# Kernel optimization log

Measured on AMD Instinct MI355X. Metric: run time of the kernel, lower is better.

Reference implementation:

```python
import jax, jax.numpy as jnp
import numpy as np

B = 1024
IN_SIZ = 16384
OUT_SIZ = 16384
C = 8          # channel_siz
NLVL = 10
IFS = IN_SIZ // 2 ** NLVL                                   # 16, in_filter_siz
KLVL = min(int(np.floor(np.log2(OUT_SIZ / 2))), NLVL)       # 10
OFS = OUT_SIZ // 2 ** KLVL                                  # 16, out_filter_siz
STD = 0.9


def setup_inputs() -> dict:
    key = jax.random.key(0)
    ks = jax.random.split(key, 2 * NLVL + 3)
    inp = {}
    inp["x"] = jax.random.normal(ks[0], (B, IN_SIZ, 1), jnp.float32)
    inp["in_filter"] = jax.random.normal(ks[1], (IFS, 1, C), jnp.float32) * STD
    inp["in_bias"] = jnp.zeros((C,), jnp.float32)
    for lvl in range(1, NLVL + 1):
        k = 2 ** lvl
        inp[f"W{lvl}"] = jax.random.normal(ks[2 * lvl], (k, 2, C, C), jnp.float32) * STD
        inp[f"b{lvl}"] = jnp.zeros((k, C), jnp.float32)
    inp["fea_dense"] = jax.random.normal(ks[-1], (2 ** KLVL, C, OFS), jnp.float32) * STD
    return inp


def _level(v, W, b):
    # v: [Kp, B, L, C] parent branches; W: [2*Kp, 2, C, C]; b: [2*Kp, C]
    # kernel-2 stride-2 conv1d: out[t] = relu(x[2t] @ W[0] + x[2t+1] @ W[1] + b)
    Kp, Bn, L, Cc = v.shape
    xp = v.reshape(Kp, Bn, L // 2, 2, Cc)
    xr = jnp.repeat(xp, 2, axis=0)  # child itk reads parent itk // 2
    y = jnp.einsum('kbtsc,kscd->kbtd', xr, W) + b[:, None, None, :]
    return jax.nn.relu(y)


def reference(x, in_filter, in_bias,
              W1, b1, W2, b2, W3, b3, W4, b4, W5, b5,
              W6, b6, W7, b7, W8, b8, W9, b9, W10, b10,
              fea_dense):
    Ws = [W1, W2, W3, W4, W5, W6, W7, W8, W9, W10]
    bs = [b1, b2, b3, b4, b5, b6, b7, b8, b9, b10]
    Bn = x.shape[0]
    # input conv1d: kernel=IFS, stride=IFS (non-overlapping) == blocked matmul
    xin = x[..., 0].reshape(Bn, 2 ** NLVL, IFS)                       # [B, 1024, 16]
    v = jax.nn.relu(jnp.einsum('bnf,fc->bnc', xin, in_filter[:, 0, :]) + in_bias)
    v = v[None]                                                        # [1, B, 1024, C]
    for lvl in range(NLVL):  # klvl == nlvl: all levels branch (tree doubling)
        v = _level(v, Ws[lvl], bs[lvl])
    # v: [2^klvl, B, 1, C] -> per-branch dense feature map
    out = jnp.einsum('kbc,kcf->bkf', v[:, :, 0, :], fea_dense)         # [B, 1024, OFS]
    return out.reshape(Bn, OUT_SIZ, 1)
```

## Files before the change

### kernel.cpp

```cpp
#include <hip/hip_runtime.h>

struct PrepPtrs { const float* W[7]; const float* Bv[7]; const float* F; const float* fb; };

__device__ __forceinline__ int cz(int c) { return c ^ ((c >> 3) & 3); }

__device__ __forceinline__ float4 relu4(float4 a) {
  return make_float4(fmaxf(a.x,0.f), fmaxf(a.y,0.f), fmaxf(a.z,0.f), fmaxf(a.w,0.f));
}
__device__ __forceinline__ void fma4(float4& acc, float s, const float4& wv) {
  acc.x = fmaf(s, wv.x, acc.x); acc.y = fmaf(s, wv.y, acc.y);
  acc.z = fmaf(s, wv.z, acc.z); acc.w = fmaf(s, wv.w, acc.w);
}

__global__ void bfly_prep(PrepPtrs P, float* __restrict__ wt) {
  int e = blockIdx.x * 256 + threadIdx.x;
  if (e >= 510 * 68) return;
  int ent = e / 68, r = e % 68, dd = r & 3;
  float v; int dst;
  if (ent < 62) {
    dst = ent * 80 + r;
    if (ent < 60) {
      int lvl, base;
      if (ent < 4)       { lvl = 1; base = 0;  }
      else if (ent < 12) { lvl = 2; base = 4;  }
      else if (ent < 28) { lvl = 3; base = 12; }
      else               { lvl = 4; base = 28; }
      int k = (ent - base) >> 1, th = ent & 1;
      if (r < 64) { int s = r >> 5, c = (r >> 2) & 7;
        v = P.W[lvl-1][k*128 + s*64 + c*8 + th*4 + dd]; }
      else v = P.Bv[lvl-1][k*8 + th*4 + dd];
    } else {
      int th = ent - 60;
      if (r < 64) { int f = r >> 2; v = P.F[f*8 + th*4 + dd]; }
      else v = P.fb[th*4 + dd];
    }
  } else {
    int eb = ent - 62;
    int q = eb / 56, rem = eb % 56;
    int lvl, Kl, base;
    if (rem < 8)       { lvl = 5; Kl = 4;  base = 0;  }
    else if (rem < 24) { lvl = 6; Kl = 8;  base = 8;  }
    else               { lvl = 7; Kl = 16; base = 24; }
    int rr = rem - base, lk = rr >> 1, th = rr & 1;
    int kg = q * Kl + lk;
    if (r < 64) { int s = r >> 5, c = (r >> 2) & 7;
      v = P.W[lvl-1][kg*128 + s*64 + c*8 + th*4 + dd]; }
    else v = P.Bv[lvl-1][kg*8 + th*4 + dd];
    dst = 4960 + eb * 80 + r;
  }
  wt[dst] = v;
}

template<int L>
__device__ __forceinline__ void ka_level(const float4* __restrict__ src,
                                         float4* __restrict__ dst,
                                         const float4* __restrict__ wt4,
                                         int lane, int wq, int th) {
  constexpr int Kc = 1 << L, Tc = 1024 >> L;
  constexpr int entBase = (Kc - 2) * 2;
  constexpr int kIters = (L <= 2) ? 1 : (1 << (L - 2));
  constexpr int tIters = 4 / kIters;
#pragma unroll
  for (int ik = 0; ik < kIters; ++ik) {
    int k;
    if constexpr (L == 1) k = wq & 1;
    else if constexpr (L == 2) k = wq;
    else k = wq + 4 * ik;
    const float4* e4 = wt4 + (entBase + k * 2 + th) * 20;
    const int kp = k >> 1;
#pragma unroll
    for (int it = 0; it < tIters; ++it) {
      int t;
      if constexpr (L == 1) t = lane + (wq >> 1) * 64 + it * 128;
      else if constexpr (L == 2) t = lane + it * 64;
      else if constexpr (L == 3) t = lane + it * 64;
      else t = lane;
      int pb = kp * (2 * Tc) + 2 * t;
      float4 A0 = src[cz(pb)],        C0 = src[cz(pb + 1)];
      float4 A1 = src[cz(pb + 1024)], C1 = src[cz(pb + 1025)];
      float4 a = e4[16];
      fma4(a, A0.x, e4[0]);  fma4(a, A0.y, e4[1]);  fma4(a, A0.z, e4[2]);  fma4(a, A0.w, e4[3]);
      fma4(a, A1.x, e4[4]);  fma4(a, A1.y, e4[5]);  fma4(a, A1.z, e4[6]);  fma4(a, A1.w, e4[7]);
      fma4(a, C0.x, e4[8]);  fma4(a, C0.y, e4[9]);  fma4(a, C0.z, e4[10]); fma4(a, C0.w, e4[11]);
      fma4(a, C1.x, e4[12]); fma4(a, C1.y, e4[13]); fma4(a, C1.z, e4[14]); fma4(a, C1.w, e4[15]);
      dst[cz(th * 1024 + k * Tc + t)] = relu4(a);
    }
  }
}

__global__ __launch_bounds__(512, 2) void bfly_ka(
    const float* __restrict__ x, const float* __restrict__ wt,
    float* __restrict__ st1)
{
  __shared__ float4 sA[2048], sB[2048];
  const int tid = threadIdx.x, b = blockIdx.x;
  const int lane = tid & 63;
  const int wv = __builtin_amdgcn_readfirstlane(tid >> 6);
  const int th = wv & 1, wq = wv >> 1;
  const float4* wt4 = (const float4*)wt;

  {
    const float4* e4 = wt4 + (60 + th) * 20;
    const float* xb = x + (size_t)b * 16384;
#pragma unroll
    for (int i = 0; i < 4; ++i) {
      int n = lane + wq * 64 + i * 256;
      const float4* xr = (const float4*)(xb + n * 16);
      float4 x0 = xr[0], x1 = xr[1], x2 = xr[2], x3 = xr[3];
      float4 a = e4[16];
      fma4(a, x0.x, e4[0]);  fma4(a, x0.y, e4[1]);  fma4(a, x0.z, e4[2]);  fma4(a, x0.w, e4[3]);
      fma4(a, x1.x, e4[4]);  fma4(a, x1.y, e4[5]);  fma4(a, x1.z, e4[6]);  fma4(a, x1.w, e4[7]);
      fma4(a, x2.x, e4[8]);  fma4(a, x2.y, e4[9]);  fma4(a, x2.z, e4[10]); fma4(a, x2.w, e4[11]);
      fma4(a, x3.x, e4[12]); fma4(a, x3.y, e4[13]); fma4(a, x3.z, e4[14]); fma4(a, x3.w, e4[15]);
      sA[cz(th * 1024 + n)] = relu4(a);
    }
  }
  __syncthreads();
  ka_level<1>(sA, sB, wt4, lane, wq, th); __syncthreads();
  ka_level<2>(sB, sA, wt4, lane, wq, th); __syncthreads();
  ka_level<3>(sA, sB, wt4, lane, wq, th); __syncthreads();
  ka_level<4>(sB, sA, wt4, lane, wq, th); __syncthreads();

  float4* o4 = (float4*)st1;
#pragma unroll
  for (int it = 0; it < 4; ++it) {
    int o = tid + it * 512;
    int t4 = o & 63, k4 = (o >> 6) & 15, h = o >> 10;
    o4[((size_t)(h * 16 + k4) * 1024 + b) * 64 + t4] = sA[cz(o)];
  }
}

template<int LV>
__device__ __forceinline__ void kb_level(const float4* __restrict__ src,
                                         float4* __restrict__ dst,
                                         const float4* __restrict__ wb4,
                                         int lane, int wv) {
  constexpr int Kc = 1 << (LV - 3);
  constexpr int Tc = 128 / Kc;
  constexpr int Tp = 256 / Kc;
  constexpr int entB = (LV == 5) ? 0 : (LV == 6) ? 8 : 24;
  constexpr int kIters = Kc / 4;
  constexpr int nIt = 4 / kIters;
  const int th = wv & 1, w2 = wv >> 1;
#pragma unroll
  for (int ik = 0; ik < kIters; ++ik) {
    const int lk = w2 + 4 * ik;
    const float4* e4 = wb4 + (entB + lk * 2 + th) * 20;
    const int lkp = lk >> 1;
#pragma unroll
    for (int it = 0; it < nIt; ++it) {
      int t, bb;
      if constexpr (LV == 5)      { t = lane & 31; bb = (lane >> 5) + it * 2; }
      else if constexpr (LV == 6) { t = lane & 15; bb = (lane >> 4) + it * 4; }
      else                        { t = lane & 7;  bb = lane >> 3; }
      int pb = bb * 256 + lkp * Tp + 2 * t;
      float4 A0 = src[cz(pb)],       C0 = src[cz(pb + 1)];
      float4 A1 = src[cz(pb + 128)], C1 = src[cz(pb + 129)];
      float4 a = e4[16];
      fma4(a, A0.x, e4[0]);  fma4(a, A0.y, e4[1]);  fma4(a, A0.z, e4[2]);  fma4(a, A0.w, e4[3]);
      fma4(a, A1.x, e4[4]);  fma4(a, A1.y, e4[5]);  fma4(a, A1.z, e4[6]);  fma4(a, A1.w, e4[7]);
      fma4(a, C0.x, e4[8]);  fma4(a, C0.y, e4[9]);  fma4(a, C0.z, e4[10]); fma4(a, C0.w, e4[11]);
      fma4(a, C1.x, e4[12]); fma4(a, C1.y, e4[13]); fma4(a, C1.z, e4[14]); fma4(a, C1.w, e4[15]);
      dst[cz(bb * 256 + th * 128 + lk * Tc + t)] = relu4(a);
    }
  }
}

__global__ __launch_bounds__(512, 2) void bfly_kb(
    const float* __restrict__ st1, const float* __restrict__ wt,
    float* __restrict__ st2)
{
  __shared__ float4 s0[2048], s1[2048];
  const int tid = threadIdx.x;
  const int q = blockIdx.x, bt = blockIdx.y;
  const int lane = tid & 63;
  const int wv = __builtin_amdgcn_readfirstlane(tid >> 6);
  const float4* wb4 = (const float4*)wt + 1240 + q * 56 * 20;
  const float4* i4 = (const float4*)st1;

#pragma unroll
  for (int it = 0; it < 4; ++it) {
    int o = tid + it * 512;
    int t4 = o & 63, lk4 = (o >> 6) & 1, h = (o >> 7) & 1, bl = o >> 8;
    float4 v = i4[((size_t)(h * 16 + 2 * q + lk4) * 1024 + bt * 8 + bl) * 64 + t4];
    s0[cz(bl * 256 + h * 128 + lk4 * 64 + t4)] = v;
  }
  __syncthreads();
  kb_level<5>(s0, s1, wb4, lane, wv); __syncthreads();
  kb_level<6>(s1, s0, wb4, lane, wv); __syncthreads();
  kb_level<7>(s0, s1, wb4, lane, wv); __syncthreads();

  float4* o4 = (float4*)st2;
#pragma unroll
  for (int it = 0; it < 4; ++it) {
    int o = tid + it * 512;
    int bl = o & 7, t7 = (o >> 3) & 7, h = (o >> 6) & 1, lk7 = o >> 7;
    float4 v = s1[cz(bl * 256 + h * 128 + lk7 * 8 + t7)];
    o4[((size_t)((16 * q + lk7) * 8 + t7) * 2 + h) * 1024 + bt * 8 + bl] = v;
  }
}

__global__ __launch_bounds__(256, 4) void bfly_kc(
    const float* __restrict__ st,
    const float* __restrict__ W8, const float* __restrict__ B8,
    const float* __restrict__ W9, const float* __restrict__ B9,
    const float* __restrict__ W10, const float* __restrict__ B10,
    const float* __restrict__ fea, float* __restrict__ out)
{
  __shared__ float4 sA[512], sB[512];
  __shared__ float swt[2928];
  const int tid = threadIdx.x;
  const int j = blockIdx.x, b0 = blockIdx.y * 32;
  const int bb = tid & 31, grp = tid >> 5;

  {
    const float4* s4 = (const float4*)st;
#pragma unroll
    for (int it = 0; it < 2; ++it) {
      int idx = tid + it * 256;
      int t = idx >> 6, h = (idx >> 5) & 1, bl = idx & 31;
      sA[h * 256 + t * 32 + bl] = s4[((size_t)((j * 8 + t) * 2 + h)) * 1024 + b0 + bl];
    }
  }
  {
    float4* d = (float4*)swt;
    for (int i = tid; i < 64;  i += 256) d[i]       = ((const float4*)(W8  + j*256 ))[i];
    for (int i = tid; i < 128; i += 256) d[64+i]    = ((const float4*)(W9  + j*512 ))[i];
    for (int i = tid; i < 256; i += 256) d[192+i]   = ((const float4*)(W10 + j*1024))[i];
    if (tid < 4)  d[448+tid] = ((const float4*)(B8  + j*16))[tid];
    if (tid < 8)  d[452+tid] = ((const float4*)(B9  + j*32))[tid];
    if (tid < 16) d[460+tid] = ((const float4*)(B10 + j*64))[tid];
    for (int i = tid; i < 256; i += 256) d[476+i]   = ((const float4*)(fea + j*1024))[i];
  }
  __syncthreads();

  auto loadW = [&](int woff, int boff, int k_l, int th, float4* w4, float4& bias) {
#pragma unroll
    for (int s = 0; s < 2; ++s)
#pragma unroll
      for (int c = 0; c < 8; ++c)
        w4[s*8+c] = *(const float4*)(swt + woff + k_l*128 + s*64 + c*8 + th*4);
    bias = *(const float4*)(swt + boff + k_l*8 + th*4);
  };
  auto mat = [&](const float4& A0, const float4& A1, const float4& C0, const float4& C1,
                 const float4* w4, float4 bias) {
    float4 a = bias;
    fma4(a, A0.x, w4[0]);  fma4(a, A0.y, w4[1]);  fma4(a, A0.z, w4[2]);  fma4(a, A0.w, w4[3]);
    fma4(a, A1.x, w4[4]);  fma4(a, A1.y, w4[5]);  fma4(a, A1.z, w4[6]);  fma4(a, A1.w, w4[7]);
    fma4(a, C0.x, w4[8]);  fma4(a, C0.y, w4[9]);  fma4(a, C0.z, w4[10]); fma4(a, C0.w, w4[11]);
    fma4(a, C1.x, w4[12]); fma4(a, C1.y, w4[13]); fma4(a, C1.z, w4[14]); fma4(a, C1.w, w4[15]);
    return relu4(a);
  };

  {
    int h = grp >> 2, k = (grp >> 1) & 1, ti = grp & 1;
    float4 w4[16], bias; loadW(0, 1792, k, h, w4, bias);
#pragma unroll
    for (int i = 0; i < 2; ++i) {
      int t = ti + 2 * i;
      float4 A0 = sA[(2*t) * 32 + bb],     A1 = sA[256 + (2*t) * 32 + bb];
      float4 C0 = sA[(2*t+1) * 32 + bb],   C1 = sA[256 + (2*t+1) * 32 + bb];
      sB[h * 256 + (2*t + k) * 32 + bb] = mat(A0, A1, C0, C1, w4, bias);
    }
  }
  __syncthreads();
  {
    int h = grp >> 2, k9 = grp & 3;
    float4 w4[16], bias; loadW(256, 1808, k9, h, w4, bias);
#pragma unroll
    for (int t9 = 0; t9 < 2; ++t9) {
      int p0 = 4 * t9 + (k9 >> 1), p1 = p0 + 2;
      float4 A0 = sB[p0 * 32 + bb], A1 = sB[256 + p0 * 32 + bb];
      float4 C0 = sB[p1 * 32 + bb], C1 = sB[256 + p1 * 32 + bb];
      sA[h * 256 + (t9 * 4 + k9) * 32 + bb] = mat(A0, A1, C0, C1, w4, bias);
    }
  }
  __syncthreads();
  {
    int k10 = grp;
    int p0 = k10 >> 1, p1 = p0 + 4;
    float4 A0 = sA[p0 * 32 + bb], A1 = sA[256 + p0 * 32 + bb];
    float4 C0 = sA[p1 * 32 + bb], C1 = sA[256 + p1 * 32 + bb];
#pragma unroll
    for (int h = 0; h < 2; ++h) {
      float4 w4[16], bias; loadW(768, 1840, k10, h, w4, bias);
      sB[h * 256 + k10 * 32 + bb] = mat(A0, A1, C0, C1, w4, bias);
    }
  }
  __syncthreads();
  {
    int ch = tid & 7, b_l = tid >> 3;
    float* op = out + ((size_t)(b0 + b_l)) * 16384 + j * 128;
#pragma unroll
    for (int it = 0; it < 4; ++it) {
      int cc = ch + it*8, k = cc >> 2, fq = cc & 3;
      float4 s0v = sB[k * 32 + b_l];
      float4 s1v = sB[256 + k * 32 + b_l];
      float sc[8] = {s0v.x,s0v.y,s0v.z,s0v.w,s1v.x,s1v.y,s1v.z,s1v.w};
      float4 acc = make_float4(0.f, 0.f, 0.f, 0.f);
#pragma unroll
      for (int c = 0; c < 8; ++c) {
        float4 fv = *(const float4*)(swt + 1904 + k*128 + c*16 + fq*4);
        acc.x = fmaf(sc[c], fv.x, acc.x); acc.y = fmaf(sc[c], fv.y, acc.y);
        acc.z = fmaf(sc[c], fv.z, acc.z); acc.w = fmaf(sc[c], fv.w, acc.w);
      }
      *(float4*)(op + k*16 + fq*4) = acc;
    }
  }
}

extern "C" void kernel_launch(void* const* d_in, const int* in_sizes, int n_in,
                              void* d_out, int out_size, void* d_ws, size_t ws_size,
                              hipStream_t stream) {
  const float* x  = (const float*)d_in[0];
  PrepPtrs P;
  P.F  = (const float*)d_in[1];
  P.fb = (const float*)d_in[2];
  for (int l = 0; l < 7; ++l) {
    P.W[l]  = (const float*)d_in[3 + 2 * l];
    P.Bv[l] = (const float*)d_in[4 + 2 * l];
  }
  const float* W8  = (const float*)d_in[17];
  const float* B8  = (const float*)d_in[18];
  const float* W9  = (const float*)d_in[19];
  const float* B9  = (const float*)d_in[20];
  const float* W10 = (const float*)d_in[21];
  const float* B10 = (const float*)d_in[22];
  const float* fea = (const float*)d_in[23];
  float* wt  = (float*)d_ws;
  float* st2 = (float*)d_ws + 65536;
  float* st1 = (float*)d_out;
  float* out = (float*)d_out;

  bfly_prep<<<dim3(136), dim3(256), 0, stream>>>(P, wt);
  bfly_ka<<<dim3(1024), dim3(512), 0, stream>>>(x, wt, st1);
  bfly_kb<<<dim3(8, 128), dim3(512), 0, stream>>>(st1, wt, st2);
  bfly_kc<<<dim3(128, 32), dim3(256), 0, stream>>>(st2, W8, B8, W9, B9, W10, B10, fea, out);
}
```

Measured before the change: 97.07 us.

## Make first butterfly stage wave-private to drop block barriers between levels

```diff
diff --git a/kernel.cpp b/kernel.cpp
--- a/kernel.cpp
+++ b/kernel.cpp
@@ -3,6 +3,7 @@
 struct PrepPtrs { const float* W[7]; const float* Bv[7]; const float* F; const float* fb; };
 
 __device__ __forceinline__ int cz(int c) { return c ^ ((c >> 3) & 3); }
+__device__ __forceinline__ int pc(int c) { return c + (c >> 3); }
 
 __device__ __forceinline__ float4 relu4(float4 a) {
   return make_float4(fmaxf(a.x,0.f), fmaxf(a.y,0.f), fmaxf(a.z,0.f), fmaxf(a.w,0.f));
@@ -52,81 +53,86 @@
 }
 
 template<int L>
-__device__ __forceinline__ void ka_level(const float4* __restrict__ src,
-                                         float4* __restrict__ dst,
+__device__ __forceinline__ void ka_level(float4* __restrict__ buf,
+                                         int srcOff, int dstOff,
                                          const float4* __restrict__ wt4,
-                                         int lane, int wq, int th) {
-  constexpr int Kc = 1 << L, Tc = 1024 >> L;
-  constexpr int entBase = (Kc - 2) * 2;
-  constexpr int kIters = (L <= 2) ? 1 : (1 << (L - 2));
-  constexpr int tIters = 4 / kIters;
-#pragma unroll
-  for (int ik = 0; ik < kIters; ++ik) {
-    int k;
-    if constexpr (L == 1) k = wq & 1;
-    else if constexpr (L == 2) k = wq;
-    else k = wq + 4 * ik;
-    const float4* e4 = wt4 + (entBase + k * 2 + th) * 20;
-    const int kp = k >> 1;
-#pragma unroll
-    for (int it = 0; it < tIters; ++it) {
-      int t;
-      if constexpr (L == 1) t = lane + (wq >> 1) * 64 + it * 128;
-      else if constexpr (L == 2) t = lane + it * 64;
-      else if constexpr (L == 3) t = lane + it * 64;
-      else t = lane;
-      int pb = kp * (2 * Tc) + 2 * t;
-      float4 A0 = src[cz(pb)],        C0 = src[cz(pb + 1)];
-      float4 A1 = src[cz(pb + 1024)], C1 = src[cz(pb + 1025)];
-      float4 a = e4[16];
-      fma4(a, A0.x, e4[0]);  fma4(a, A0.y, e4[1]);  fma4(a, A0.z, e4[2]);  fma4(a, A0.w, e4[3]);
-      fma4(a, A1.x, e4[4]);  fma4(a, A1.y, e4[5]);  fma4(a, A1.z, e4[6]);  fma4(a, A1.w, e4[7]);
-      fma4(a, C0.x, e4[8]);  fma4(a, C0.y, e4[9]);  fma4(a, C0.z, e4[10]); fma4(a, C0.w, e4[11]);
-      fma4(a, C1.x, e4[12]); fma4(a, C1.y, e4[13]); fma4(a, C1.z, e4[14]); fma4(a, C1.w, e4[15]);
-      dst[cz(th * 1024 + k * Tc + t)] = relu4(a);
-    }
-  }
-}
-
-__global__ __launch_bounds__(512, 2) void bfly_ka(
+                                         int lane) {
+  constexpr int K = 1 << L;
+  constexpr int T = 128 >> L;
+  constexpr int G = 32 >> L;
+  const int kth = lane / G, tg = lane % G;
+  const int k = kth >> 1, th = kth & 1;
+  const int kp = k >> 1;
+  const float4* e4 = wt4 + (((K - 2) * 2 + k * 2 + th) * 20);
+  float4 w0 = e4[0],  w1 = e4[1],  w2 = e4[2],  w3 = e4[3];
+  float4 w4_ = e4[4], w5 = e4[5],  w6 = e4[6],  w7 = e4[7];
+  float4 w8 = e4[8],  w9 = e4[9],  w10 = e4[10], w11 = e4[11];
+  float4 w12 = e4[12], w13 = e4[13], w14 = e4[14], w15 = e4[15];
+  const float4 bias = e4[16];
+#pragma unroll
+  for (int it = 0; it < 4; ++it) {
+    int t = tg + it * G;
+    int pr = kp * (2 * T) + 2 * t;
+    float4 A0 = buf[srcOff + pc(pr)];
+    float4 A1 = buf[srcOff + pc(128 + pr)];
+    float4 C0 = buf[srcOff + pc(pr + 1)];
+    float4 C1 = buf[srcOff + pc(128 + pr + 1)];
+    float4 a = bias;
+    fma4(a, A0.x, w0);  fma4(a, A0.y, w1);  fma4(a, A0.z, w2);  fma4(a, A0.w, w3);
+    fma4(a, A1.x, w4_); fma4(a, A1.y, w5);  fma4(a, A1.z, w6);  fma4(a, A1.w, w7);
+    fma4(a, C0.x, w8);  fma4(a, C0.y, w9);  fma4(a, C0.z, w10); fma4(a, C0.w, w11);
+    fma4(a, C1.x, w12); fma4(a, C1.y, w13); fma4(a, C1.z, w14); fma4(a, C1.w, w15);
+    buf[dstOff + pc(th * 128 + k * T + t)] = relu4(a);
+  }
+}
+
+__global__ __launch_bounds__(256, 4) void bfly_ka(
     const float* __restrict__ x, const float* __restrict__ wt,
     float* __restrict__ st1)
 {
-  __shared__ float4 sA[2048], sB[2048];
-  const int tid = threadIdx.x, b = blockIdx.x;
+  __shared__ float4 lds[4 * 2 * 288];
+  const int tid = threadIdx.x;
+  const int b = blockIdx.x >> 1, hb = blockIdx.x & 1;
   const int lane = tid & 63;
-  const int wv = __builtin_amdgcn_readfirstlane(tid >> 6);
-  const int th = wv & 1, wq = wv >> 1;
+  const int wv = tid >> 6;
   const float4* wt4 = (const float4*)wt;
+  float4* buf = lds + wv * 576;
 
   {
+    const int th = lane >> 5, ng = lane & 31;
     const float4* e4 = wt4 + (60 + th) * 20;
-    const float* xb = x + (size_t)b * 16384;
+    float4 f0 = e4[0],  f1 = e4[1],  f2 = e4[2],  f3 = e4[3];
+    float4 f4_ = e4[4], f5 = e4[5],  f6 = e4[6],  f7 = e4[7];
+    float4 f8 = e4[8],  f9 = e4[9],  f10 = e4[10], f11 = e4[11];
+    float4 f12 = e4[12], f13 = e4[13], f14 = e4[14], f15 = e4[15];
+    const float4 bias = e4[16];
+    const float* xb = x + (size_t)b * 16384 + (hb * 512 + wv * 128) * 16;
 #pragma unroll
     for (int i = 0; i < 4; ++i) {
-      int n = lane + wq * 64 + i * 256;
+      int n = ng + i * 32;
       const float4* xr = (const float4*)(xb + n * 16);
       float4 x0 = xr[0], x1 = xr[1], x2 = xr[2], x3 = xr[3];
-      float4 a = e4[16];
-      fma4(a, x0.x, e4[0]);  fma4(a, x0.y, e4[1]);  fma4(a, x0.z, e4[2]);  fma4(a, x0.w, e4[3]);
-      fma4(a, x1.x, e4[4]);  fma4(a, x1.y, e4[5]);  fma4(a, x1.z, e4[6]);  fma4(a, x1.w, e4[7]);
-      fma4(a, x2.x, e4[8]);  fma4(a, x2.y, e4[9]);  fma4(a, x2.z, e4[10]); fma4(a, x2.w, e4[11]);
-      fma4(a, x3.x, e4[12]); fma4(a, x3.y, e4[13]); fma4(a, x3.z, e4[14]); fma4(a, x3.w, e4[15]);
-      sA[cz(th * 1024 + n)] = relu4(a);
-    }
-  }
-  __syncthreads();
-  ka_level<1>(sA, sB, wt4, lane, wq, th); __syncthreads();
-  ka_level<2>(sB, sA, wt4, lane, wq, th); __syncthreads();
-  ka_level<3>(sA, sB, wt4, lane, wq, th); __syncthreads();
-  ka_level<4>(sB, sA, wt4, lane, wq, th); __syncthreads();
+      float4 a = bias;
+      fma4(a, x0.x, f0);  fma4(a, x0.y, f1);  fma4(a, x0.z, f2);  fma4(a, x0.w, f3);
+      fma4(a, x1.x, f4_); fma4(a, x1.y, f5);  fma4(a, x1.z, f6);  fma4(a, x1.w, f7);
+      fma4(a, x2.x, f8);  fma4(a, x2.y, f9);  fma4(a, x2.z, f10); fma4(a, x2.w, f11);
+      fma4(a, x3.x, f12); fma4(a, x3.y, f13); fma4(a, x3.z, f14); fma4(a, x3.w, f15);
+      buf[pc(th * 128 + n)] = relu4(a);
+    }
+  }
+  ka_level<1>(buf, 0, 288, wt4, lane);
+  ka_level<2>(buf, 288, 0, wt4, lane);
+  ka_level<3>(buf, 0, 288, wt4, lane);
+  ka_level<4>(buf, 288, 0, wt4, lane);
+  __syncthreads();
 
   float4* o4 = (float4*)st1;
 #pragma unroll
   for (int it = 0; it < 4; ++it) {
-    int o = tid + it * 512;
-    int t4 = o & 63, k4 = (o >> 6) & 15, h = o >> 10;
-    o4[((size_t)(h * 16 + k4) * 1024 + b) * 64 + t4] = sA[cz(o)];
+    int idx = tid + it * 256;
+    int t4b = idx & 31, k4 = (idx >> 5) & 15, h = idx >> 9;
+    float4 v = lds[(t4b >> 3) * 576 + pc(h * 128 + k4 * 8 + (t4b & 7))];
+    o4[((size_t)(h * 16 + k4) * 1024 + b) * 64 + hb * 32 + t4b] = v;
   }
 }
 
@@ -252,8 +258,7 @@
     return relu4(a);
   };
 
-  {
-    int h = grp >> 2, k = (grp >> 1) & 1, ti = grp & 1;
+  { int h = grp >> 2, k = (grp >> 1) & 1, ti = grp & 1;
     float4 w4[16], bias; loadW(0, 1792, k, h, w4, bias);
 #pragma unroll
     for (int i = 0; i < 2; ++i) {
@@ -264,8 +269,7 @@
     }
   }
   __syncthreads();
-  {
-    int h = grp >> 2, k9 = grp & 3;
+  { int h = grp >> 2, k9 = grp & 3;
     float4 w4[16], bias; loadW(256, 1808, k9, h, w4, bias);
 #pragma unroll
     for (int t9 = 0; t9 < 2; ++t9) {
@@ -276,8 +280,7 @@
     }
   }
   __syncthreads();
-  {
-    int k10 = grp;
+  { int k10 = grp;
     int p0 = k10 >> 1, p1 = p0 + 4;
     float4 A0 = sA[p0 * 32 + bb], A1 = sA[256 + p0 * 32 + bb];
     float4 C0 = sA[p1 * 32 + bb], C1 = sA[256 + p1 * 32 + bb];
@@ -288,8 +291,7 @@
     }
   }
   __syncthreads();
-  {
-    int ch = tid & 7, b_l = tid >> 3;
+  { int ch = tid & 7, b_l = tid >> 3;
     float* op = out + ((size_t)(b0 + b_l)) * 16384 + j * 128;
 #pragma unroll
     for (int it = 0; it < 4; ++it) {
@@ -333,7 +335,7 @@
   float* out = (float*)d_out;
 
   bfly_prep<<<dim3(136), dim3(256), 0, stream>>>(P, wt);
-  bfly_ka<<<dim3(1024), dim3(512), 0, stream>>>(x, wt, st1);
+  bfly_ka<<<dim3(2048), dim3(256), 0, stream>>>(x, wt, st1);
   bfly_kb<<<dim3(8, 128), dim3(512), 0, stream>>>(st1, wt, st2);
   bfly_kc<<<dim3(128, 32), dim3(256), 0, stream>>>(st2, W8, B8, W9, B9, W10, B10, fea, out);
 }
```

Result: no change. 96.46 us (-0.6%).
